# Kernel tuning notes

Hardware: AMD Instinct MI355X
Metric: run time of the kernel (lower is better)

The kernel has to match this reference:

```python
import jax, jax.numpy as jnp
import numpy as np

N = 50000          # nodes
E = 1600000        # edges (avg degree 32)
C_E = 64           # edge feature channels
C_N = 256          # node feature channels
C_OUT = 256        # output channels


def setup_inputs() -> dict:
    key = jax.random.key(0)
    ks = jax.random.split(key, 8)
    D = jax.random.uniform(ks[0], (N,), dtype=jnp.float32) + 0.5  # degree-like, bounded away from 0
    row_idx = jax.random.randint(ks[1], (E,), 0, N)               # destination node of each edge
    edge_attr = jax.random.normal(ks[2], (E, C_E), dtype=jnp.float32)
    X = jax.random.normal(ks[3], (N, C_N), dtype=jnp.float32)
    # learned params (nn.Linear: y = x @ W.T + b); store transposed for x @ W
    W_pass = jax.random.normal(ks[4], (C_E, C_OUT), dtype=jnp.float32) / np.sqrt(C_E)
    b_pass = jax.random.normal(ks[5], (C_OUT,), dtype=jnp.float32) * 0.01
    W_self = jax.random.normal(ks[6], (C_N, C_OUT), dtype=jnp.float32) / np.sqrt(C_N)
    b_self = jax.random.normal(ks[7], (C_OUT,), dtype=jnp.float32) * 0.01
    return {"D": D, "row_idx": row_idx, "edge_attr": edge_attr, "X": X,
            "W_pass": W_pass, "b_pass": b_pass, "W_self": W_self, "b_self": b_self}


def reference(D, row_idx, edge_attr, X, W_pass, b_pass, W_self, b_self):
    # torch.sparse.sum(A, dim=1).to_dense(): sum edge features into their row node -> (N, C_E)
    A = jax.ops.segment_sum(edge_attr, row_idx, num_segments=D.shape[0])
    # pass_map(A / D[:, None]) + self_map(X), then ReLU
    out = (A / D[:, None]) @ W_pass + b_pass + X @ W_self + b_self
    return jax.nn.relu(out)
```

## Files before the change

kernel.cpp:

```cpp
#include <hip/hip_runtime.h>
#include <hip/hip_bf16.h>

#define NNODES 50000
#define NEDGES 1600000
#define CE 64
#define CN 256
#define COUT 256
#define KTOT (CE + CN)
#define BCAP 64

#define FBM 128
#define FBN 256
#define FBK 32
#define PAD 8

typedef __attribute__((ext_vector_type(8))) short bf16x8;
typedef __attribute__((ext_vector_type(4))) float f32x4;

__device__ inline ushort f2bf(float f) {
    __hip_bfloat16 h = __float2bfloat16(f);
    return *(ushort*)&h;
}

__global__ __launch_bounds__(256) void fill_kernel(
    const int* __restrict__ row_idx,
    const float* __restrict__ ea,
    int* __restrict__ counts,
    int* __restrict__ buckets,
    float* __restrict__ Aovf)
{
    int e = blockIdx.x * 256 + threadIdx.x;
    int r = row_idx[e];
    int pos = atomicAdd(&counts[r], 1);
    if (pos < BCAP) {
        buckets[r * BCAP + pos] = e;
    } else {
        for (int c = 0; c < CE; ++c)
            atomicAdd(&Aovf[r * CE + c], ea[e * CE + c]);
    }
}

__global__ __launch_bounds__(256) void prep_kernel(
    const float* __restrict__ Wp, const float* __restrict__ Ws,
    const float* __restrict__ bp, const float* __restrict__ bs,
    ushort* __restrict__ Wt, float* __restrict__ bias)
{
    int k = blockIdx.x;
    int n = threadIdx.x;
    float v = (k < CE) ? Wp[k * COUT + n] : Ws[(k - CE) * COUT + n];
    Wt[n * KTOT + k] = f2bf(v);
    if (k == 0) bias[n] = bp[n] + bs[n];
}

__global__ __launch_bounds__(256, 2) void fused_kernel(
    const float4* __restrict__ ea4,
    const int* __restrict__ counts,
    const int* __restrict__ buckets,
    const float* __restrict__ D,
    const float4* __restrict__ Aovf4,
    const float* __restrict__ X,
    const ushort* __restrict__ Wt,
    const float* __restrict__ bias,
    float* __restrict__ out)
{
    __shared__ ushort sAg0[FBM][FBK + PAD];
    __shared__ ushort sAg1[FBM][FBK + PAD];
    __shared__ ushort sX [FBM][FBK + PAD];
    __shared__ ushort sB [FBN][FBK + PAD];

    const int tid  = threadIdx.x;
    const int wave = tid >> 6;
    const int lane = tid & 63;
    const int row0 = blockIdx.x * FBM;

    {
        const int sub = lane >> 4;
        const int c4  = lane & 15;

        const int nb  = row0 + wave * 32 + (lane & 31);
        const int nbc = (nb < NNODES) ? nb : (NNODES - 1);
        const int   cntv = counts[nbc];
        const float dvv  = D[nbc];

        for (int lm = 0; lm < 32; ++lm) {
            const int m = wave * 32 + lm;
            const int n = row0 + m;
            const int cshf = __shfl(cntv, lm);
            const int rawdeg = (n < NNODES) ? cshf : 0;
            const int deg = (rawdeg < BCAP) ? rawdeg : BCAP;

            float4 a0 = make_float4(0.f, 0.f, 0.f, 0.f);
            float4 a1 = make_float4(0.f, 0.f, 0.f, 0.f);
            int bktv = 0;
            if (n < NNODES) bktv = buckets[(size_t)n * BCAP + lane];

            int i = 0;
            for (; i + 8 <= deg; i += 8) {
                const int e0 = __shfl(bktv, i + sub);
                const int e1 = __shfl(bktv, i + 4 + sub);
                const float4 v0 = ea4[(size_t)e0 * 16 + c4];
                const float4 v1 = ea4[(size_t)e1 * 16 + c4];
                a0.x += v0.x; a0.y += v0.y; a0.z += v0.z; a0.w += v0.w;
                a1.x += v1.x; a1.y += v1.y; a1.z += v1.z; a1.w += v1.w;
            }
            for (; i < deg; i += 4) {
                const int e0 = __shfl(bktv, i + sub);
                if (i + sub < deg) {
                    const float4 v0 = ea4[(size_t)e0 * 16 + c4];
                    a0.x += v0.x; a0.y += v0.y; a0.z += v0.z; a0.w += v0.w;
                }
            }

            a0.x += a1.x; a0.y += a1.y; a0.z += a1.z; a0.w += a1.w;
            a0.x += __shfl_xor(a0.x, 16); a0.x += __shfl_xor(a0.x, 32);
            a0.y += __shfl_xor(a0.y, 16); a0.y += __shfl_xor(a0.y, 32);
            a0.z += __shfl_xor(a0.z, 16); a0.z += __shfl_xor(a0.z, 32);
            a0.w += __shfl_xor(a0.w, 16); a0.w += __shfl_xor(a0.w, 32);

            const float dv = __shfl(dvv, lm);
            if (sub == 0) {
                const float invd = (n < NNODES) ? (1.0f / dv) : 0.f;
                float4 prev = make_float4(0.f, 0.f, 0.f, 0.f);
                if (n < NNODES && rawdeg > BCAP)
                    prev = Aovf4[(size_t)n * 16 + c4];
                ushort4 o;
                o.x = f2bf((a0.x + prev.x) * invd);
                o.y = f2bf((a0.y + prev.y) * invd);
                o.z = f2bf((a0.z + prev.z) * invd);
                o.w = f2bf((a0.w + prev.w) * invd);
                ushort* dst = (c4 < 8) ? &sAg0[m][c4 * 4] : &sAg1[m][(c4 - 8) * 4];
                *(ushort4*)dst = o;
            }
        }
    }

    const int m16 = lane & 15;
    const int kg  = lane >> 4;
    const int wr  = (wave >> 1) * 64;
    const int wc  = (wave & 1) * 128;
    const int sr  = tid >> 1;
    const int sh  = tid & 1;
    const int brr = tid >> 2;
    const int bq  = tid & 3;

    f32x4 acc[4][8];
    #pragma unroll
    for (int i = 0; i < 4; ++i)
        #pragma unroll
        for (int j = 0; j < 8; ++j)
            acc[i][j] = (f32x4){0.f, 0.f, 0.f, 0.f};

    #pragma unroll
    for (int ks = 0; ks < KTOT / FBK; ++ks) {
        const int k0 = ks * FBK;

        #pragma unroll
        for (int p = 0; p < 4; ++p) {
            const int r = brr + p * 64;
            const uint4 v = *(const uint4*)(Wt + (size_t)r * KTOT + k0 + bq * 8);
            *(uint4*)&sB[r][bq * 8] = v;
        }

        if (ks >= 2) {
            const int gn = row0 + sr;
            uint4 v0 = {0, 0, 0, 0}, v1 = {0, 0, 0, 0};
            if (gn < NNODES) {
                const float4* xs = (const float4*)(X + (size_t)gn * CN + (k0 - CE) + sh * 16);
                const float4 a = xs[0], b = xs[1], c = xs[2], d = xs[3];
                union { ushort us[8]; uint4 u; } p0, p1;
                p0.us[0]=f2bf(a.x); p0.us[1]=f2bf(a.y); p0.us[2]=f2bf(a.z); p0.us[3]=f2bf(a.w);
                p0.us[4]=f2bf(b.x); p0.us[5]=f2bf(b.y); p0.us[6]=f2bf(b.z); p0.us[7]=f2bf(b.w);
                p1.us[0]=f2bf(c.x); p1.us[1]=f2bf(c.y); p1.us[2]=f2bf(c.z); p1.us[3]=f2bf(c.w);
                p1.us[4]=f2bf(d.x); p1.us[5]=f2bf(d.y); p1.us[6]=f2bf(d.z); p1.us[7]=f2bf(d.w);
                v0 = p0.u; v1 = p1.u;
            }
            *(uint4*)&sX[sr][sh * 16]     = v0;
            *(uint4*)&sX[sr][sh * 16 + 8] = v1;
        }
        __syncthreads();

        const ushort (*sa)[FBK + PAD] = (ks == 0) ? sAg0 : (ks == 1) ? sAg1 : sX;
        bf16x8 aF[4];
        #pragma unroll
        for (int i = 0; i < 4; ++i)
            aF[i] = *(const bf16x8*)&sa[wr + i * 16 + m16][kg * 8];
        #pragma unroll
        for (int j = 0; j < 8; ++j) {
            const bf16x8 bFj = *(const bf16x8*)&sB[wc + j * 16 + m16][kg * 8];
            #pragma unroll
            for (int i = 0; i < 4; ++i)
                acc[i][j] = __builtin_amdgcn_mfma_f32_16x16x32_bf16(aF[i], bFj, acc[i][j], 0, 0, 0);
        }
        __syncthreads();
    }

    #pragma unroll
    for (int j = 0; j < 8; ++j) {
        const int col = wc + j * 16 + m16;
        const float bv = bias[col];
        #pragma unroll
        for (int i = 0; i < 4; ++i) {
            const int rbase = row0 + wr + i * 16 + kg * 4;
            #pragma unroll
            for (int t = 0; t < 4; ++t) {
                const int row = rbase + t;
                if (row < NNODES)
                    out[(size_t)row * COUT + col] = fmaxf(acc[i][j][t] + bv, 0.f);
            }
        }
    }
}

extern "C" void kernel_launch(void* const* d_in, const int* in_sizes, int n_in,
                              void* d_out, int out_size, void* d_ws, size_t ws_size,
                              hipStream_t stream) {
    const float* D         = (const float*)d_in[0];
    const int*   row_idx   = (const int*)  d_in[1];
    const float* edge_attr = (const float*)d_in[2];
    const float* X         = (const float*)d_in[3];
    const float* W_pass    = (const float*)d_in[4];
    const float* b_pass    = (const float*)d_in[5];
    const float* W_self    = (const float*)d_in[6];
    const float* b_self    = (const float*)d_in[7];
    float* out = (float*)d_out;

    char* ws = (char*)d_ws;
    size_t off = 0;
    float* Aovf   = (float*)(ws + off); off += (size_t)NNODES * CE * 4;
    int*   counts = (int*)  (ws + off); off += (size_t)NNODES * 4;
    int*   buckets= (int*)  (ws + off); off += (size_t)NNODES * BCAP * 4;
    ushort* Wt    = (ushort*)(ws + off); off += (size_t)COUT * KTOT * 2;
    float* bias   = (float*)(ws + off); off += (size_t)COUT * 4;

    hipMemsetAsync(Aovf, 0, (size_t)NNODES * CE * sizeof(float), stream);
    hipMemsetAsync(counts, 0, (size_t)NNODES * sizeof(int), stream);

    fill_kernel<<<dim3(NEDGES / 256), dim3(256), 0, stream>>>(
        row_idx, edge_attr, counts, buckets, Aovf);

    prep_kernel<<<dim3(KTOT), dim3(256), 0, stream>>>(
        W_pass, W_self, b_pass, b_self, Wt, bias);

    fused_kernel<<<dim3((NNODES + FBM - 1) / FBM), dim3(256), 0, stream>>>(
        (const float4*)edge_attr, counts, buckets, D, (const float4*)Aovf,
        X, Wt, bias, out);
}
```

Measured before the change: 801.6 us.

## Split fused gather+GEMM into separate gather kernel and MFMA GEMM kernel

Moves the edge gather/segment-sum out of the fused kernel into its own kernel that uses one wave per node across 12500 blocks. Each node's normalized aggregate is written as bf16 to a workspace buffer, and the GEMM kernel reads it like the X tiles. The gather also unrolls to four independent accumulators to keep more loads in flight. This aims to raise parallelism and latency hiding for the irregular gather, which was serialized 32 nodes per wave ahead of the GEMM in the fused kernel. The cost is an extra launch and a round trip of a 6.4MB intermediate through global memory.

Result: faster. 775.8 us (-3.2%).

```diff
diff --git a/kernel.cpp b/kernel.cpp
--- a/kernel.cpp
+++ b/kernel.cpp
@@ -9,9 +9,9 @@
 #define KTOT (CE + CN)
 #define BCAP 64
 
-#define FBM 128
-#define FBN 256
-#define FBK 32
+#define GBM 128
+#define GBN 256
+#define GBK 32
 #define PAD 8
 
 typedef __attribute__((ext_vector_type(8))) short bf16x8;
@@ -52,96 +52,102 @@
     if (k == 0) bias[n] = bp[n] + bs[n];
 }
 
-__global__ __launch_bounds__(256, 2) void fused_kernel(
+__global__ __launch_bounds__(256) void gather_kernel(
     const float4* __restrict__ ea4,
     const int* __restrict__ counts,
     const int* __restrict__ buckets,
     const float* __restrict__ D,
     const float4* __restrict__ Aovf4,
+    ushort* __restrict__ Abf)
+{
+    const int wave = threadIdx.x >> 6;
+    const int lane = threadIdx.x & 63;
+    const int n = blockIdx.x * 4 + wave;
+    const int sub = lane >> 4;
+    const int c4  = lane & 15;
+
+    const int rawdeg = counts[n];
+    const int deg = (rawdeg < BCAP) ? rawdeg : BCAP;
+    const int bktv = buckets[(size_t)n * BCAP + lane];
+
+    float4 a0 = make_float4(0.f,0.f,0.f,0.f);
+    float4 a1 = make_float4(0.f,0.f,0.f,0.f);
+    float4 a2 = make_float4(0.f,0.f,0.f,0.f);
+    float4 a3 = make_float4(0.f,0.f,0.f,0.f);
+
+    int i = 0;
+    for (; i + 16 <= deg; i += 16) {
+        const int e0 = __shfl(bktv, i + sub);
+        const int e1 = __shfl(bktv, i + 4  + sub);
+        const int e2 = __shfl(bktv, i + 8  + sub);
+        const int e3 = __shfl(bktv, i + 12 + sub);
+        const float4 v0 = ea4[(size_t)e0 * 16 + c4];
+        const float4 v1 = ea4[(size_t)e1 * 16 + c4];
+        const float4 v2 = ea4[(size_t)e2 * 16 + c4];
+        const float4 v3 = ea4[(size_t)e3 * 16 + c4];
+        a0.x += v0.x; a0.y += v0.y; a0.z += v0.z; a0.w += v0.w;
+        a1.x += v1.x; a1.y += v1.y; a1.z += v1.z; a1.w += v1.w;
+        a2.x += v2.x; a2.y += v2.y; a2.z += v2.z; a2.w += v2.w;
+        a3.x += v3.x; a3.y += v3.y; a3.z += v3.z; a3.w += v3.w;
+    }
+    for (; i + 4 <= deg; i += 4) {
+        const int e0 = __shfl(bktv, i + sub);
+        const float4 v0 = ea4[(size_t)e0 * 16 + c4];
+        a0.x += v0.x; a0.y += v0.y; a0.z += v0.z; a0.w += v0.w;
+    }
+    if (i < deg) {
+        const int e0 = __shfl(bktv, i + sub);
+        if (i + sub < deg) {
+            const float4 v0 = ea4[(size_t)e0 * 16 + c4];
+            a0.x += v0.x; a0.y += v0.y; a0.z += v0.z; a0.w += v0.w;
+        }
+    }
+
+    a0.x += a1.x + a2.x + a3.x;
+    a0.y += a1.y + a2.y + a3.y;
+    a0.z += a1.z + a2.z + a3.z;
+    a0.w += a1.w + a2.w + a3.w;
+    a0.x += __shfl_xor(a0.x, 16); a0.x += __shfl_xor(a0.x, 32);
+    a0.y += __shfl_xor(a0.y, 16); a0.y += __shfl_xor(a0.y, 32);
+    a0.z += __shfl_xor(a0.z, 16); a0.z += __shfl_xor(a0.z, 32);
+    a0.w += __shfl_xor(a0.w, 16); a0.w += __shfl_xor(a0.w, 32);
+
+    if (sub == 0) {
+        const float invd = 1.0f / D[n];
+        float4 prev = make_float4(0.f,0.f,0.f,0.f);
+        if (rawdeg > BCAP)
+            prev = Aovf4[(size_t)n * 16 + c4];
+        ushort4 o;
+        o.x = f2bf((a0.x + prev.x) * invd);
+        o.y = f2bf((a0.y + prev.y) * invd);
+        o.z = f2bf((a0.z + prev.z) * invd);
+        o.w = f2bf((a0.w + prev.w) * invd);
+        *(ushort4*)&Abf[(size_t)n * CE + c4 * 4] = o;
+    }
+}
+
+__global__ __launch_bounds__(256, 2) void mfma_gemm_kernel(
+    const ushort* __restrict__ Abf,
     const float* __restrict__ X,
     const ushort* __restrict__ Wt,
     const float* __restrict__ bias,
     float* __restrict__ out)
 {
-    __shared__ ushort sAg0[FBM][FBK + PAD];
-    __shared__ ushort sAg1[FBM][FBK + PAD];
-    __shared__ ushort sX [FBM][FBK + PAD];
-    __shared__ ushort sB [FBN][FBK + PAD];
+    __shared__ ushort sA[GBM][GBK + PAD];
+    __shared__ ushort sB[GBN][GBK + PAD];
 
     const int tid  = threadIdx.x;
     const int wave = tid >> 6;
     const int lane = tid & 63;
-    const int row0 = blockIdx.x * FBM;
-
-    {
-        const int sub = lane >> 4;
-        const int c4  = lane & 15;
-
-        const int nb  = row0 + wave * 32 + (lane & 31);
-        const int nbc = (nb < NNODES) ? nb : (NNODES - 1);
-        const int   cntv = counts[nbc];
-        const float dvv  = D[nbc];
-
-        for (int lm = 0; lm < 32; ++lm) {
-            const int m = wave * 32 + lm;
-            const int n = row0 + m;
-            const int cshf = __shfl(cntv, lm);
-            const int rawdeg = (n < NNODES) ? cshf : 0;
-            const int deg = (rawdeg < BCAP) ? rawdeg : BCAP;
-
-            float4 a0 = make_float4(0.f, 0.f, 0.f, 0.f);
-            float4 a1 = make_float4(0.f, 0.f, 0.f, 0.f);
-            int bktv = 0;
-            if (n < NNODES) bktv = buckets[(size_t)n * BCAP + lane];
-
-            int i = 0;
-            for (; i + 8 <= deg; i += 8) {
-                const int e0 = __shfl(bktv, i + sub);
-                const int e1 = __shfl(bktv, i + 4 + sub);
-                const float4 v0 = ea4[(size_t)e0 * 16 + c4];
-                const float4 v1 = ea4[(size_t)e1 * 16 + c4];
-                a0.x += v0.x; a0.y += v0.y; a0.z += v0.z; a0.w += v0.w;
-                a1.x += v1.x; a1.y += v1.y; a1.z += v1.z; a1.w += v1.w;
-            }
-            for (; i < deg; i += 4) {
-                const int e0 = __shfl(bktv, i + sub);
-                if (i + sub < deg) {
-                    const float4 v0 = ea4[(size_t)e0 * 16 + c4];
-                    a0.x += v0.x; a0.y += v0.y; a0.z += v0.z; a0.w += v0.w;
-                }
-            }
-
-            a0.x += a1.x; a0.y += a1.y; a0.z += a1.z; a0.w += a1.w;
-            a0.x += __shfl_xor(a0.x, 16); a0.x += __shfl_xor(a0.x, 32);
-            a0.y += __shfl_xor(a0.y, 16); a0.y += __shfl_xor(a0.y, 32);
-            a0.z += __shfl_xor(a0.z, 16); a0.z += __shfl_xor(a0.z, 32);
-            a0.w += __shfl_xor(a0.w, 16); a0.w += __shfl_xor(a0.w, 32);
-
-            const float dv = __shfl(dvv, lm);
-            if (sub == 0) {
-                const float invd = (n < NNODES) ? (1.0f / dv) : 0.f;
-                float4 prev = make_float4(0.f, 0.f, 0.f, 0.f);
-                if (n < NNODES && rawdeg > BCAP)
-                    prev = Aovf4[(size_t)n * 16 + c4];
-                ushort4 o;
-                o.x = f2bf((a0.x + prev.x) * invd);
-                o.y = f2bf((a0.y + prev.y) * invd);
-                o.z = f2bf((a0.z + prev.z) * invd);
-                o.w = f2bf((a0.w + prev.w) * invd);
-                ushort* dst = (c4 < 8) ? &sAg0[m][c4 * 4] : &sAg1[m][(c4 - 8) * 4];
-                *(ushort4*)dst = o;
-            }
-        }
-    }
-
-    const int m16 = lane & 15;
-    const int kg  = lane >> 4;
-    const int wr  = (wave >> 1) * 64;
-    const int wc  = (wave & 1) * 128;
-    const int sr  = tid >> 1;
-    const int sh  = tid & 1;
-    const int brr = tid >> 2;
-    const int bq  = tid & 3;
+    const int row0 = blockIdx.x * GBM;
+    const int m16  = lane & 15;
+    const int kg   = lane >> 4;
+    const int wr   = (wave >> 1) * 64;
+    const int wc   = (wave & 1) * 128;
+    const int sr   = tid >> 1;
+    const int sh   = tid & 1;
+    const int brr  = tid >> 2;
+    const int bq   = tid & 3;
 
     f32x4 acc[4][8];
     #pragma unroll
@@ -151,8 +157,8 @@
             acc[i][j] = (f32x4){0.f, 0.f, 0.f, 0.f};
 
     #pragma unroll
-    for (int ks = 0; ks < KTOT / FBK; ++ks) {
-        const int k0 = ks * FBK;
+    for (int ks = 0; ks < KTOT / GBK; ++ks) {
+        const int k0 = ks * GBK;
 
         #pragma unroll
         for (int p = 0; p < 4; ++p) {
@@ -161,29 +167,33 @@
             *(uint4*)&sB[r][bq * 8] = v;
         }
 
-        if (ks >= 2) {
+        {
             const int gn = row0 + sr;
-            uint4 v0 = {0, 0, 0, 0}, v1 = {0, 0, 0, 0};
+            uint4 v0 = {0,0,0,0}, v1 = {0,0,0,0};
             if (gn < NNODES) {
-                const float4* xs = (const float4*)(X + (size_t)gn * CN + (k0 - CE) + sh * 16);
-                const float4 a = xs[0], b = xs[1], c = xs[2], d = xs[3];
-                union { ushort us[8]; uint4 u; } p0, p1;
-                p0.us[0]=f2bf(a.x); p0.us[1]=f2bf(a.y); p0.us[2]=f2bf(a.z); p0.us[3]=f2bf(a.w);
-                p0.us[4]=f2bf(b.x); p0.us[5]=f2bf(b.y); p0.us[6]=f2bf(b.z); p0.us[7]=f2bf(b.w);
-                p1.us[0]=f2bf(c.x); p1.us[1]=f2bf(c.y); p1.us[2]=f2bf(c.z); p1.us[3]=f2bf(c.w);
-                p1.us[4]=f2bf(d.x); p1.us[5]=f2bf(d.y); p1.us[6]=f2bf(d.z); p1.us[7]=f2bf(d.w);
-                v0 = p0.u; v1 = p1.u;
+                if (ks < 2) {
+                    const uint4* src = (const uint4*)(Abf + (size_t)gn * CE + k0 + sh * 16);
+                    v0 = src[0]; v1 = src[1];
+                } else {
+                    const float4* xs = (const float4*)(X + (size_t)gn * CN + (k0 - CE) + sh * 16);
+                    const float4 a = xs[0], b = xs[1], c = xs[2], d = xs[3];
+                    union { ushort us[8]; uint4 u; } p0, p1;
+                    p0.us[0]=f2bf(a.x); p0.us[1]=f2bf(a.y); p0.us[2]=f2bf(a.z); p0.us[3]=f2bf(a.w);
+                    p0.us[4]=f2bf(b.x); p0.us[5]=f2bf(b.y); p0.us[6]=f2bf(b.z); p0.us[7]=f2bf(b.w);
+                    p1.us[0]=f2bf(c.x); p1.us[1]=f2bf(c.y); p1.us[2]=f2bf(c.z); p1.us[3]=f2bf(c.w);
+                    p1.us[4]=f2bf(d.x); p1.us[5]=f2bf(d.y); p1.us[6]=f2bf(d.z); p1.us[7]=f2bf(d.w);
+                    v0 = p0.u; v1 = p1.u;
+                }
             }
-            *(uint4*)&sX[sr][sh * 16]     = v0;
-            *(uint4*)&sX[sr][sh * 16 + 8] = v1;
+            *(uint4*)&sA[sr][sh * 16]     = v0;
+            *(uint4*)&sA[sr][sh * 16 + 8] = v1;
         }
         __syncthreads();
 
-        const ushort (*sa)[FBK + PAD] = (ks == 0) ? sAg0 : (ks == 1) ? sAg1 : sX;
         bf16x8 aF[4];
         #pragma unroll
         for (int i = 0; i < 4; ++i)
-            aF[i] = *(const bf16x8*)&sa[wr + i * 16 + m16][kg * 8];
+            aF[i] = *(const bf16x8*)&sA[wr + i * 16 + m16][kg * 8];
         #pragma unroll
         for (int j = 0; j < 8; ++j) {
             const bf16x8 bFj = *(const bf16x8*)&sB[wc + j * 16 + m16][kg * 8];
@@ -229,6 +239,7 @@
     float* Aovf   = (float*)(ws + off); off += (size_t)NNODES * CE * 4;
     int*   counts = (int*)  (ws + off); off += (size_t)NNODES * 4;
     int*   buckets= (int*)  (ws + off); off += (size_t)NNODES * BCAP * 4;
+    ushort* Abf   = (ushort*)(ws + off); off += (size_t)NNODES * CE * 2;
     ushort* Wt    = (ushort*)(ws + off); off += (size_t)COUT * KTOT * 2;
     float* bias   = (float*)(ws + off); off += (size_t)COUT * 4;
 
@@ -241,7 +252,9 @@
     prep_kernel<<<dim3(KTOT), dim3(256), 0, stream>>>(
         W_pass, W_self, b_pass, b_self, Wt, bias);
 
-    fused_kernel<<<dim3((NNODES + FBM - 1) / FBM), dim3(256), 0, stream>>>(
-        (const float4*)edge_attr, counts, buckets, D, (const float4*)Aovf,
-        X, Wt, bias, out);
-}
+    gather_kernel<<<dim3(NNODES / 4), dim3(256), 0, stream>>>(
+        (const float4*)edge_attr, counts, buckets, D, (const float4*)Aovf, Abf);
+
+    mfma_gemm_kernel<<<dim3((NNODES + GBM - 1) / GBM), dim3(256), 0, stream>>>(
+        Abf, X, Wt, bias, out);
+}
```
